# Performance work log

Measured on AMD Instinct MI355X. Metric: run time of the kernel, lower is better.

## Reference

```python
import jax, jax.numpy as jnp
import numpy as np

B, S, D, E, H = 4, 2048, 1024, 8, 2048


def setup_inputs() -> dict:
    key = jax.random.key(0)
    ks = jax.random.split(key, 8)
    s_in = 1.0 / np.sqrt(D)   # torch Linear default init scale (uniform bound)
    s_hid = 1.0 / np.sqrt(H)
    return {
        "x": jax.random.normal(ks[0], (B, S, D), dtype=jnp.float32),
        "W1": jax.random.uniform(ks[1], (E, D, H), minval=-s_in, maxval=s_in, dtype=jnp.float32),
        "b1": jax.random.uniform(ks[2], (E, H), minval=-s_in, maxval=s_in, dtype=jnp.float32),
        "W2": jax.random.uniform(ks[3], (E, H, D), minval=-s_hid, maxval=s_hid, dtype=jnp.float32),
        "b2": jax.random.uniform(ks[4], (E, D), minval=-s_hid, maxval=s_hid, dtype=jnp.float32),
        "Wg": jax.random.uniform(ks[5], (D, E), minval=-s_in, maxval=s_in, dtype=jnp.float32),
        "bg": jax.random.uniform(ks[6], (E,), minval=-s_in, maxval=s_in, dtype=jnp.float32),
    }


def reference(x, W1, b1, W2, b2, Wg, bg):
    # All-experts dense MoE (eval mode: dropout is identity).
    # hidden: [B,S,E,H]
    h = jax.nn.relu(jnp.einsum("bsd,edh->bseh", x, W1) + b1)
    # expert outputs: [B,S,E,D]
    expert_out = jnp.einsum("bseh,ehd->bsed", h, W2) + b2
    # gate (raw linear, no softmax in original): [B,S,E]
    gate = jnp.einsum("bsd,de->bse", x, Wg) + bg
    # gate-weighted sum over experts -> [B,S,D]
    return jnp.einsum("bse,bsed->bsd", gate, expert_out)
```

## Files before the change

kernel.cpp:

```cpp
#include <hip/hip_runtime.h>

#define NTOK 8192
#define DDIM 1024
#define HDIM 2048
#define NEXP 8
#define G1_NKT 16

typedef unsigned short u16;
typedef short bf16x8 __attribute__((ext_vector_type(8)));
typedef float f32x4 __attribute__((ext_vector_type(4)));
typedef float float4_t __attribute__((ext_vector_type(4)));

__device__ __forceinline__ u16 f2bf(float f) {
  unsigned u = __float_as_uint(f);
  u += 0x7FFFu + ((u >> 16) & 1u);
  return (u16)(u >> 16);
}

#define GLOAD_LDS16(gp, lp)                                                     \
  __builtin_amdgcn_global_load_lds(                                             \
      (const __attribute__((address_space(1))) unsigned int*)(gp),              \
      (__attribute__((address_space(3))) unsigned int*)(lp), 16, 0, 0)

#define VMW(n) asm volatile("s_waitcnt vmcnt(" #n ")" ::: "memory")
#define ENTRYB()                                                                \
  { __builtin_amdgcn_s_barrier(); __builtin_amdgcn_sched_barrier(0); }

__global__ void k_prep(const float* __restrict__ x, const float* __restrict__ Wg,
                       const float* __restrict__ bg,
                       u16* __restrict__ xb, float* __restrict__ gate) {
  const int tok = (blockIdx.x * 256 + threadIdx.x) >> 6;
  const int lane = threadIdx.x & 63;
  const float* xr = x + (size_t)tok * DDIM;
  u16* xo = xb + (size_t)tok * DDIM;
  float s[NEXP];
#pragma unroll
  for (int e = 0; e < NEXP; ++e) s[e] = 0.f;
#pragma unroll
  for (int it = 0; it < 2; ++it) {
    const int d0 = lane * 8 + it * 512;
    float4_t v0 = *(const float4_t*)(xr + d0);
    float4_t v1 = *(const float4_t*)(xr + d0 + 4);
    union { bf16x8 v; u16 h[8]; } u;
    u.h[0] = f2bf(v0.x); u.h[1] = f2bf(v0.y); u.h[2] = f2bf(v0.z); u.h[3] = f2bf(v0.w);
    u.h[4] = f2bf(v1.x); u.h[5] = f2bf(v1.y); u.h[6] = f2bf(v1.z); u.h[7] = f2bf(v1.w);
    *(bf16x8*)(xo + d0) = u.v;
    float xv[8] = {v0.x, v0.y, v0.z, v0.w, v1.x, v1.y, v1.z, v1.w};
#pragma unroll
    for (int j = 0; j < 8; ++j) {
      const float4_t w0 = *(const float4_t*)(Wg + (size_t)(d0 + j) * NEXP);
      const float4_t w1 = *(const float4_t*)(Wg + (size_t)(d0 + j) * NEXP + 4);
      s[0] += xv[j] * w0.x; s[1] += xv[j] * w0.y;
      s[2] += xv[j] * w0.z; s[3] += xv[j] * w0.w;
      s[4] += xv[j] * w1.x; s[5] += xv[j] * w1.y;
      s[6] += xv[j] * w1.z; s[7] += xv[j] * w1.w;
    }
  }
#pragma unroll
  for (int off = 32; off; off >>= 1)
#pragma unroll
    for (int e = 0; e < NEXP; ++e) s[e] += __shfl_down(s[e], off);
  if (lane == 0) {
#pragma unroll
    for (int e = 0; e < NEXP; ++e) gate[(size_t)tok * NEXP + e] = s[e] + bg[e];
  }
}

__global__ void k_transpose(const float* __restrict__ in, u16* __restrict__ out,
                            int R, int C, size_t oexp, int orstride) {
  __shared__ float t[64][65];
  const int rb = blockIdx.x * 64, cb = blockIdx.y * 64;
  const float* pin = in + (size_t)blockIdx.z * R * C;
  u16* pout = out + (size_t)blockIdx.z * oexp;
  const int tid = threadIdx.x;
  {
    const int r = tid >> 4;
    const int c4 = (tid & 15) * 4;
#pragma unroll
    for (int i = 0; i < 4; ++i) {
      float4_t v = *(const float4_t*)(pin + (size_t)(rb + r + 16 * i) * C + cb + c4);
      t[r + 16 * i][c4 + 0] = v.x;
      t[r + 16 * i][c4 + 1] = v.y;
      t[r + 16 * i][c4 + 2] = v.z;
      t[r + 16 * i][c4 + 3] = v.w;
    }
  }
  __syncthreads();
  {
    const int oc = tid >> 3;
    const int r8 = (tid & 7) * 8;
#pragma unroll
    for (int jp = 0; jp < 2; ++jp) {
      const int ocol = oc + 32 * jp;
      union { bf16x8 v; u16 h[8]; } u;
#pragma unroll
      for (int k = 0; k < 8; ++k) u.h[k] = f2bf(t[r8 + k][ocol]);
      *(bf16x8*)(pout + (size_t)(cb + ocol) * orstride + rb + r8) = u.v;
    }
  }
}

__global__ __launch_bounds__(512, 2) void k_g1(
    const u16* __restrict__ A, const u16* __restrict__ Bt,
    const float* __restrict__ bias, const float* __restrict__ gate,
    int ebase, u16* __restrict__ Cout, int KW, int ca, int cgcols) {
  __shared__ __align__(16) u16 lds[65536];
  const int tid = threadIdx.x, lane = tid & 63, wid = tid >> 6;
  const int wm = wid >> 2, wn = wid & 3;
  const int wg = blockIdx.x;
  const int xcd = wg & 7, lo = wg >> 3;
  const int cr = xcd / cgcols, cc = xcd % cgcols;
  const int tm = cr * ca + (lo >> 3);
  const int tn = cc * 8 + (lo & 7);
  const int bm = tm * 256, bn = tn * 256;

  const int srow = tid >> 3;
  const int scol = ((tid & 7) ^ (srow & 7)) << 3;
  const u16* gA = A + (size_t)(bm + srow) * 1024 + scol;
  const u16* gB = Bt + (size_t)(bn + srow) * 1024 + scol;
  const int dofs = wid * 512;

  u16* aB0 = lds;          u16* bB0 = lds + 16384;
  u16* aB1 = lds + 32768;  u16* bB1 = lds + 49152;

  const int fr = lane & 15, fq = lane >> 4, xr = fr & 7;
  const int so0 = ((0 + fq) ^ xr) << 3;
  const int so1 = ((4 + fq) ^ xr) << 3;

  f32x4 acc[4][4][2] = {};
  bf16x8 av[4][2], bv[2][2];

#define G1_SA(dst, hh, ts)                                                      \
  { GLOAD_LDS16(gA + (size_t)((hh)*128     ) * 1024 + (size_t)(ts) * 64,        \
                (dst) + ((hh)*128     ) * 64 + dofs);                           \
    GLOAD_LDS16(gA + (size_t)((hh)*128 + 64) * 1024 + (size_t)(ts) * 64,        \
                (dst) + ((hh)*128 + 64) * 64 + dofs); }
#define G1_SB(dst, hh, ts)                                                      \
  { GLOAD_LDS16(gB + (size_t)((hh)*128     ) * 1024 + (size_t)(ts) * 64,        \
                (dst) + ((hh)*128     ) * 64 + dofs);                           \
    GLOAD_LDS16(gB + (size_t)((hh)*128 + 64) * 1024 + (size_t)(ts) * 64,        \
                (dst) + ((hh)*128 + 64) * 64 + dofs); }
#define RD_A_K(src, MH, KK)                                                     \
  { _Pragma("unroll") for (int i_ = 0; i_ < 4; ++i_) {                          \
      const int rb_ = ((MH)*128 + wm * 64 + i_ * 16 + fr) << 6;                 \
      av[i_][KK] = *(const bf16x8*)((src) + rb_ + ((KK) ? so1 : so0)); } }
#define RD_B_K(src, NH, KK)                                                     \
  { _Pragma("unroll") for (int n_ = 0; n_ < 2; ++n_) {                          \
      const int rb_ = ((NH)*128 + wn * 32 + n_ * 16 + fr) << 6;                 \
      bv[n_][KK] = *(const bf16x8*)((src) + rb_ + ((KK) ? so1 : so0)); } }
#define MMA16(Q)                                                                \
  { __builtin_amdgcn_s_setprio(1);                                              \
    _Pragma("unroll") for (int k_ = 0; k_ < 2; ++k_)                            \
    _Pragma("unroll") for (int i_ = 0; i_ < 4; ++i_)                            \
    _Pragma("unroll") for (int n_ = 0; n_ < 2; ++n_)                            \
      acc[Q][i_][n_] = __builtin_amdgcn_mfma_f32_16x16x32_bf16(                 \
          av[i_][k_], bv[n_][k_], acc[Q][i_][n_], 0, 0, 0);                     \
    __builtin_amdgcn_s_setprio(0); }

  G1_SA(aB0, 0, 0); G1_SB(bB0, 0, 0); G1_SA(aB0, 1, 0); G1_SB(bB0, 1, 0);

  u16 *aC_ = aB0, *bC_ = bB0, *aN_ = aB1, *bN_ = bB1;

#pragma unroll 1
  for (int t = 0; t < G1_NKT; ++t) {
    const bool s1 = (t + 1 < G1_NKT);
    VMW(4); ENTRYB();
    RD_A_K(aC_, 0, 0); RD_B_K(bC_, 0, 0);
    RD_A_K(aC_, 0, 1); RD_B_K(bC_, 0, 1);
    if (s1) G1_SA(aN_, 0, t + 1);
    MMA16(0);
    if (s1) { VMW(4); } else { VMW(2); }
    ENTRYB();
    RD_A_K(aC_, 1, 0); RD_A_K(aC_, 1, 1);
    if (s1) G1_SB(bN_, 0, t + 1);
    MMA16(2);
    if (s1) { VMW(4); } else { VMW(0); }
    ENTRYB();
    RD_B_K(bC_, 1, 0); RD_B_K(bC_, 1, 1);
    if (s1) G1_SA(aN_, 1, t + 1);
    MMA16(3);
    RD_A_K(aC_, 0, 0); RD_A_K(aC_, 0, 1);
    if (s1) G1_SB(bN_, 1, t + 1);
    MMA16(1);
    u16* tp;
    tp = aC_; aC_ = aN_; aN_ = tp;
    tp = bC_; bC_ = bN_; bN_ = tp;
  }

#pragma unroll
  for (int q = 0; q < 4; ++q) {
    const int MH = q >> 1, NH = q & 1;
    const int cb0 = bn + NH * 128 + wn * 32;
    const int e = ebase + (cb0 >> 11);
    float bcol[2];
#pragma unroll
    for (int n = 0; n < 2; ++n) bcol[n] = bias[cb0 + n * 16 + fr];
#pragma unroll
    for (int i = 0; i < 4; ++i) {
#pragma unroll
      for (int j = 0; j < 4; ++j) {
        const int r = bm + MH * 128 + wm * 64 + i * 16 + fq * 4 + j;
        const float g = gate[(size_t)r * NEXP + e];
#pragma unroll
        for (int n = 0; n < 2; ++n) {
          float v = fmaxf(acc[q][i][n][j] + bcol[n], 0.f) * g;
          Cout[(size_t)r * KW + cb0 + n * 16 + fr] = f2bf(v);
        }
      }
    }
  }
#undef G1_SA
#undef G1_SB
#undef RD_A_K
#undef RD_B_K
#undef MMA16
}

__global__ __launch_bounds__(512, 2) void k_g2(
    const u16* __restrict__ A, const u16* __restrict__ Bt,
    const float* __restrict__ bias, const float* __restrict__ gate,
    float* __restrict__ Cout, int accum, int KW, int nk) {
  __shared__ __align__(16) u16 lds[49152];
  const int tid = threadIdx.x, lane = tid & 63, wid = tid >> 6;
  const int wm = wid >> 2, wn = wid & 3;
  const int wg = blockIdx.x;
  const int xcd = wg & 7, lo = wg >> 3;
  const int tm = xcd * 8 + (lo >> 2);
  const int tn = lo & 3;
  const int bm = tm * 128, bn = tn * 256;

  const int srow = tid >> 3;
  const int scol = ((tid & 7) ^ (srow & 7)) << 3;
  const u16* gA = A + (size_t)(bm + srow) * KW + scol;
  const u16* gB = Bt + (size_t)(bn + srow) * HDIM + scol;
  const int dofs = wid * 512;

  u16* aB0 = lds;          u16* bB0 = lds + 8192;
  u16* aB1 = lds + 24576;  u16* bB1 = lds + 32768;

  const int fr = lane & 15, fq = lane >> 4, xr = fr & 7;
  const int so0 = ((0 + fq) ^ xr) << 3;
  const int so1 = ((4 + fq) ^ xr) << 3;

  f32x4 acc[2][4][2] = {};
  bf16x8 av[4][2], bv[2][2];

#define G2_BOFF(ts) ((size_t)((ts) >> 5) * ((size_t)DDIM * HDIM) +              \
                     (size_t)((ts) & 31) * 64)
#define G2_SA(dst, ts)                                                          \
  { GLOAD_LDS16(gA + (size_t)(ts) * 64, (dst) + dofs);                          \
    GLOAD_LDS16(gA + (size_t)64 * KW + (size_t)(ts) * 64,                       \
                (dst) + 4096 + dofs); }
#define G2_SB(dst, hh, ts)                                                      \
  { GLOAD_LDS16(gB + (size_t)((hh)*128     ) * HDIM + G2_BOFF(ts),              \
                (dst) + ((hh)*128     ) * 64 + dofs);                           \
    GLOAD_LDS16(gB + (size_t)((hh)*128 + 64) * HDIM + G2_BOFF(ts),              \
                (dst) + ((hh)*128 + 64) * 64 + dofs); }
#define G2_RDA_K(src, KK)                                                       \
  { _Pragma("unroll") for (int i_ = 0; i_ < 4; ++i_) {                          \
      const int rb_ = (wm * 64 + i_ * 16 + fr) << 6;                            \
      av[i_][KK] = *(const bf16x8*)((src) + rb_ + ((KK) ? so1 : so0)); } }
#define G2_RDB_K(src, NH, KK)                                                   \
  { _Pragma("unroll") for (int n_ = 0; n_ < 2; ++n_) {                          \
      const int rb_ = ((NH)*128 + wn * 32 + n_ * 16 + fr) << 6;                 \
      bv[n_][KK] = *(const bf16x8*)((src) + rb_ + ((KK) ? so1 : so0)); } }
#define G2_MMA(Q)                                                               \
  { __builtin_amdgcn_s_setprio(1);                                              \
    _Pragma("unroll") for (int k_ = 0; k_ < 2; ++k_)                            \
    _Pragma("unroll") for (int i_ = 0; i_ < 4; ++i_)                            \
    _Pragma("unroll") for (int n_ = 0; n_ < 2; ++n_)                            \
      acc[Q][i_][n_] = __builtin_amdgcn_mfma_f32_16x16x32_bf16(                 \
          av[i_][k_], bv[n_][k_], acc[Q][i_][n_], 0, 0, 0);                     \
    __builtin_amdgcn_s_setprio(0); }

  G2_SA(aB0, 0); G2_SB(bB0, 0, 0); G2_SB(bB0, 1, 0);

  u16 *aC_ = aB0, *bC_ = bB0, *aN_ = aB1, *bN_ = bB1;

#pragma unroll 1
  for (int t = 0; t < nk; ++t) {
    const bool s1 = (t + 1 < nk);
    VMW(2); ENTRYB();
    G2_RDA_K(aC_, 0); G2_RDB_K(bC_, 0, 0);
    G2_RDA_K(aC_, 1); G2_RDB_K(bC_, 0, 1);
    if (s1) { G2_SA(aN_, t + 1); G2_SB(bN_, 0, t + 1); }
    G2_MMA(0);
    if (s1) { VMW(4); } else { VMW(0); }
    ENTRYB();
    G2_RDB_K(bC_, 1, 0); G2_RDB_K(bC_, 1, 1);
    if (s1) G2_SB(bN_, 1, t + 1);
    G2_MMA(1);
    u16* tp;
    tp = aC_; aC_ = aN_; aN_ = tp;
    tp = bC_; bC_ = bN_; bN_ = tp;
  }

  float b2c[2][2][NEXP];
  if (!accum) {
#pragma unroll
    for (int nh = 0; nh < 2; ++nh)
#pragma unroll
      for (int n = 0; n < 2; ++n)
#pragma unroll
        for (int e = 0; e < NEXP; ++e)
          b2c[nh][n][e] = bias[(size_t)e * DDIM + bn + nh * 128 + wn * 32 + n * 16 + fr];
  }
#pragma unroll
  for (int NH = 0; NH < 2; ++NH) {
    const int cb0 = bn + NH * 128 + wn * 32;
#pragma unroll
    for (int i = 0; i < 4; ++i) {
#pragma unroll
      for (int j = 0; j < 4; ++j) {
        const int r = bm + wm * 64 + i * 16 + fq * 4 + j;
        if (!accum) {
          float g8[NEXP];
#pragma unroll
          for (int e = 0; e < NEXP; ++e) g8[e] = gate[(size_t)r * NEXP + e];
#pragma unroll
          for (int n = 0; n < 2; ++n) {
            float v = acc[NH][i][n][j];
#pragma unroll
            for (int e = 0; e < NEXP; ++e) v += g8[e] * b2c[NH][n][e];
            Cout[(size_t)r * DDIM + cb0 + n * 16 + fr] = v;
          }
        } else {
#pragma unroll
          for (int n = 0; n < 2; ++n) {
            const size_t idx = (size_t)r * DDIM + cb0 + n * 16 + fr;
            Cout[idx] += acc[NH][i][n][j];
          }
        }
      }
    }
  }
#undef G2_BOFF
#undef G2_SA
#undef G2_SB
#undef G2_RDA_K
#undef G2_RDB_K
#undef G2_MMA
}

extern "C" void kernel_launch(void* const* d_in, const int* in_sizes, int n_in,
                              void* d_out, int out_size, void* d_ws, size_t ws_size,
                              hipStream_t stream) {
  (void)in_sizes; (void)n_in; (void)out_size;
  const float* x  = (const float*)d_in[0];
  const float* W1 = (const float*)d_in[1];
  const float* b1 = (const float*)d_in[2];
  const float* W2 = (const float*)d_in[3];
  const float* b2 = (const float*)d_in[4];
  const float* Wg = (const float*)d_in[5];
  const float* bg = (const float*)d_in[6];
  float* out = (float*)d_out;

  size_t o_xb   = 0;
  size_t o_w1t  = o_xb  + (size_t)NTOK * DDIM * 2;
  size_t o_w2t  = o_w1t + (size_t)NEXP * HDIM * DDIM * 2;
  size_t o_gate = o_w2t + (size_t)NEXP * DDIM * HDIM * 2;
  size_t o_h    = o_gate + (size_t)NTOK * NEXP * 4;

  int G = 4;
  if (o_h + (size_t)NTOK * G * HDIM * 2 > ws_size) G = 2;
  if (o_h + (size_t)NTOK * G * HDIM * 2 > ws_size) return;

  u16*   xb   = (u16*)((char*)d_ws + o_xb);
  u16*   W1t  = (u16*)((char*)d_ws + o_w1t);
  u16*   W2t  = (u16*)((char*)d_ws + o_w2t);
  float* gate = (float*)((char*)d_ws + o_gate);
  u16*   hbuf = (u16*)((char*)d_ws + o_h);

  k_prep<<<NTOK / 4, 256, 0, stream>>>(x, Wg, bg, xb, gate);
  dim3 g1(DDIM / 64, HDIM / 64, NEXP);
  k_transpose<<<g1, 256, 0, stream>>>(W1, W1t, DDIM, HDIM, (size_t)HDIM * DDIM, DDIM);
  dim3 g2(HDIM / 64, DDIM / 64, NEXP);
  k_transpose<<<g2, 256, 0, stream>>>(W2, W2t, HDIM, DDIM, (size_t)DDIM * HDIM, HDIM);

  const int KW = G * HDIM;
  const int ca1 = (G == 4) ? 16 : 8;
  const int cg1 = (G == 4) ? 4 : 2;
  for (int g = 0; g < NEXP / G; ++g) {
    k_g1<<<(NTOK / 256) * (KW / 256), 512, 0, stream>>>(
        xb, W1t + (size_t)g * KW * DDIM,
        b1 + (size_t)g * KW, gate, g * G, hbuf, KW, ca1, cg1);
    k_g2<<<256, 512, 0, stream>>>(
        hbuf, W2t + (size_t)g * G * DDIM * HDIM,
        b2, gate, out, g > 0, KW, KW / 64);
  }
}
```

Baseline: 589.5 us.

## Software-pipeline GEMM2 MMA halves across iterations with double-buffered fragment registers

Restructures the GEMM2 main loop so the second-half MFMA block of iteration t runs in iteration t+1, after that iteration's LDS reads are issued, using ping-pong A-fragment registers and separate B-fragment registers. The loop is unrolled by two so buffer pointers are compile-time and need no swapping. The aim is to hide LDS read latency and barrier stalls behind MFMA work, at the cost of more VGPRs (possibly lower occupancy). It also assumes nk is even.

Measured after the change: 583.0 us. Within noise of the previous version (-1.1%).

```diff
diff --git a/kernel.cpp b/kernel.cpp
--- a/kernel.cpp
+++ b/kernel.cpp
@@ -243,7 +243,7 @@
   const int so1 = ((4 + fq) ^ xr) << 3;
 
   f32x4 acc[2][4][2] = {};
-  bf16x8 av[4][2], bv[2][2];
+  bf16x8 avA[8], avB[8], bv0[2][2], bv1[2][2];
 
 #define G2_BOFF(ts) ((size_t)((ts) >> 5) * ((size_t)DDIM * HDIM) +              \
                      (size_t)((ts) & 31) * 64)
@@ -256,44 +256,47 @@
                 (dst) + ((hh)*128     ) * 64 + dofs);                           \
     GLOAD_LDS16(gB + (size_t)((hh)*128 + 64) * HDIM + G2_BOFF(ts),              \
                 (dst) + ((hh)*128 + 64) * 64 + dofs); }
-#define G2_RDA_K(src, KK)                                                       \
+#define G2_RDA_TO(DST, src)                                                     \
   { _Pragma("unroll") for (int i_ = 0; i_ < 4; ++i_) {                          \
       const int rb_ = (wm * 64 + i_ * 16 + fr) << 6;                            \
-      av[i_][KK] = *(const bf16x8*)((src) + rb_ + ((KK) ? so1 : so0)); } }
-#define G2_RDB_K(src, NH, KK)                                                   \
+      (DST)[i_ * 2 + 0] = *(const bf16x8*)((src) + rb_ + so0);                  \
+      (DST)[i_ * 2 + 1] = *(const bf16x8*)((src) + rb_ + so1); } }
+#define G2_RDB_TO(DST, src, NH)                                                 \
   { _Pragma("unroll") for (int n_ = 0; n_ < 2; ++n_) {                          \
       const int rb_ = ((NH)*128 + wn * 32 + n_ * 16 + fr) << 6;                 \
-      bv[n_][KK] = *(const bf16x8*)((src) + rb_ + ((KK) ? so1 : so0)); } }
-#define G2_MMA(Q)                                                               \
+      (DST)[n_][0] = *(const bf16x8*)((src) + rb_ + so0);                       \
+      (DST)[n_][1] = *(const bf16x8*)((src) + rb_ + so1); } }
+#define G2_MMA(Q, AV, BV)                                                       \
   { __builtin_amdgcn_s_setprio(1);                                              \
     _Pragma("unroll") for (int k_ = 0; k_ < 2; ++k_)                            \
     _Pragma("unroll") for (int i_ = 0; i_ < 4; ++i_)                            \
     _Pragma("unroll") for (int n_ = 0; n_ < 2; ++n_)                            \
       acc[Q][i_][n_] = __builtin_amdgcn_mfma_f32_16x16x32_bf16(                 \
-          av[i_][k_], bv[n_][k_], acc[Q][i_][n_], 0, 0, 0);                     \
+          (AV)[i_ * 2 + k_], (BV)[n_][k_], acc[Q][i_][n_], 0, 0, 0);            \
     __builtin_amdgcn_s_setprio(0); }
 
+#define G2_ITER(T, AV, AVP, aCur, bCur, aNx, bNx)                               \
+  {                                                                             \
+    VMW(2); ENTRYB();                                                           \
+    G2_RDA_TO(AV, aCur);                                                        \
+    G2_RDB_TO(bv0, bCur, 0);                                                    \
+    if ((T) + 1 < nk) { G2_SA(aNx, (T) + 1); G2_SB(bNx, 0, (T) + 1); }          \
+    if ((T) > 0) G2_MMA(1, AVP, bv1);                                           \
+    if ((T) + 1 < nk) { VMW(4); } else { VMW(0); }                              \
+    ENTRYB();                                                                   \
+    G2_RDB_TO(bv1, bCur, 1);                                                    \
+    if ((T) + 1 < nk) G2_SB(bNx, 1, (T) + 1);                                   \
+    G2_MMA(0, AV, bv0);                                                         \
+  }
+
   G2_SA(aB0, 0); G2_SB(bB0, 0, 0); G2_SB(bB0, 1, 0);
 
-  u16 *aC_ = aB0, *bC_ = bB0, *aN_ = aB1, *bN_ = bB1;
-
 #pragma unroll 1
-  for (int t = 0; t < nk; ++t) {
-    const bool s1 = (t + 1 < nk);
-    VMW(2); ENTRYB();
-    G2_RDA_K(aC_, 0); G2_RDB_K(bC_, 0, 0);
-    G2_RDA_K(aC_, 1); G2_RDB_K(bC_, 0, 1);
-    if (s1) { G2_SA(aN_, t + 1); G2_SB(bN_, 0, t + 1); }
-    G2_MMA(0);
-    if (s1) { VMW(4); } else { VMW(0); }
-    ENTRYB();
-    G2_RDB_K(bC_, 1, 0); G2_RDB_K(bC_, 1, 1);
-    if (s1) G2_SB(bN_, 1, t + 1);
-    G2_MMA(1);
-    u16* tp;
-    tp = aC_; aC_ = aN_; aN_ = tp;
-    tp = bC_; bC_ = bN_; bN_ = tp;
-  }
+  for (int tt = 0; tt < nk; tt += 2) {
+    G2_ITER(tt,     avA, avB, aB0, bB0, aB1, bB1);
+    G2_ITER(tt + 1, avB, avA, aB1, bB1, aB0, bB0);
+  }
+  G2_MMA(1, avB, bv1);
 
   float b2c[2][2][NEXP];
   if (!accum) {
@@ -337,9 +340,10 @@
 #undef G2_BOFF
 #undef G2_SA
 #undef G2_SB
-#undef G2_RDA_K
-#undef G2_RDB_K
+#undef G2_RDA_TO
+#undef G2_RDB_TO
 #undef G2_MMA
+#undef G2_ITER
 }
 
 extern "C" void kernel_launch(void* const* d_in, const int* in_sizes, int n_in,
```
